# Performance work log

Measured on AMD Instinct MI355X. Metric: run time of the kernel, lower is better.

The kernel has to match this reference:

```python
import jax, jax.numpy as jnp
import numpy as np

B, H, W, C = 64, 14, 14, 768
HID = 4 * C            # ConvNeXt MLP hidden
E, K, R = 8, 2, 16     # num_experts, top_k, lora rank
SCALING = 16.0 / 16.0  # alpha / r


def setup_inputs() -> dict:
    key = jax.random.key(0)
    ks = jax.random.split(key, 9)
    N = B * H * W
    x = jax.random.normal(ks[0], (B, H, W, C), jnp.float32)
    p = jax.random.uniform(ks[1], (N, K), jnp.float32)
    topk_probs = p / (p.sum(-1, keepdims=True) + 1e-6)
    topk_idx = jax.random.randint(ks[2], (N, K), 0, E)
    w1 = jax.random.normal(ks[3], (C, HID), jnp.float32) * (C ** -0.5)
    b1 = jnp.zeros((HID,), jnp.float32)
    w2 = jax.random.normal(ks[4], (HID, C), jnp.float32) * (HID ** -0.5)
    b2 = jnp.zeros((C,), jnp.float32)
    w_down = jax.random.normal(ks[5], (E, C, R), jnp.float32) * (C ** -0.5)
    # torch init is zeros; use small randn so the op is numerically non-trivial
    w_up = jax.random.normal(ks[6], (E, R, C), jnp.float32) * 0.02
    return {"x": x, "topk_probs": topk_probs, "topk_idx": topk_idx,
            "w1": w1, "b1": b1, "w2": w2, "b2": b2,
            "w_down": w_down, "w_up": w_up}


def reference(x, topk_probs, topk_idx, w1, b1, w2, b2, w_down, w_up):
    # orig ConvNeXt MLP: Linear -> GELU(exact) -> Linear, pointwise over [B,H,W,C]
    h = jax.nn.gelu(jnp.einsum('bhwc,cf->bhwf', x, w1) + b1, approximate=False)
    orig = jnp.einsum('bhwf,fc->bhwc', h, w2) + b2

    N = x.shape[0] * x.shape[1] * x.shape[2]
    xf = x.reshape(N, C)  # [N, C] tokens
    # per-token combine weight for each expert: sum_k p[n,k] * 1[idx[n,k]==e]
    wt = (jax.nn.one_hot(topk_idx, E, dtype=xf.dtype) * topk_probs[..., None]).sum(1)  # [N, E]
    # dense-over-experts LoRA (vectorized form of the per-expert gather/scatter loop)
    down = jax.nn.gelu(jnp.einsum('nc,ecr->ner', xf, w_down), approximate=False)  # [N, E, R]
    up = jnp.einsum('ner,erc->nec', down, w_up) * SCALING                          # [N, E, C]
    moe = jnp.einsum('nec,ne->nc', up, wt)                                         # [N, C]
    return orig + moe.reshape(x.shape)
```

## Files before the change

### kernel.cpp

```cpp
#include <hip/hip_runtime.h>
#include <hip/hip_bf16.h>
#include <math.h>


#define NTOK   12544
#define CDIM   768
#define HIDDIM 3072
#define KBIG   3200

typedef __attribute__((ext_vector_type(8))) short bf16x8;
typedef __attribute__((ext_vector_type(4))) float f32x4;

#define GLOBAL_AS(p) ((const __attribute__((address_space(1))) void*)(p))
#define LDS_AS(p)    ((__attribute__((address_space(3))) void*)(p))
#define GLD(src, dst) __builtin_amdgcn_global_load_lds(GLOBAL_AS(src), LDS_AS(dst), 16, 0, 0)

__device__ inline unsigned short f2bf(float f) {
    unsigned int x = __float_as_uint(f);
    x += 0x7fffu + ((x >> 16) & 1u);
    return (unsigned short)(x >> 16);
}

__device__ inline float gelu_fast(float x) {
    float x3 = x * x * x;
    float u2 = 1.5957691216057308f * x + 0.07135481627260025f * x3;
    float e = __expf(-u2);
    return x * __builtin_amdgcn_rcpf(1.0f + e);
}

__global__ void __launch_bounds__(256) prep_kernel(
        const float* __restrict__ x, const float* __restrict__ w1,
        const float* __restrict__ w2, const float* __restrict__ wup,
        const float* __restrict__ wdn,
        unsigned short* __restrict__ xb, unsigned short* __restrict__ w1t,
        unsigned short* __restrict__ B2t, unsigned short* __restrict__ wdt) {
    __shared__ float tile[64][65];
    const int b = blockIdx.x, tid = threadIdx.x;
    if (b < 9408) {
        int i = b * 256 + tid;
        float4 v = ((const float4*)x)[i];
        ushort4 o;
        o.x = f2bf(v.x); o.y = f2bf(v.y); o.z = f2bf(v.z); o.w = f2bf(v.w);
        ((ushort4*)xb)[i] = o;
        return;
    }
    if (b < 10584) {
        const float* in; unsigned short* outp; int Ccols, out_ld, out_off, bx, by;
        if (b < 9984)       { int t = b - 9408;  in = w1;  outp = w1t; Ccols = 3072; out_ld = 768;  out_off = 0;    bx = t % 48; by = t / 48; }
        else if (b < 10560) { int t = b - 9984;  in = w2;  outp = B2t; Ccols = 768;  out_ld = 3200; out_off = 0;    bx = t % 12; by = t / 12; }
        else                { int t = b - 10560; in = wup; outp = B2t; Ccols = 768;  out_ld = 3200; out_off = 3072; bx = t % 12; by = t / 12; }
        const int c0 = bx * 64, r0 = by * 64;
        #pragma unroll
        for (int p = 0; p < 4; ++p) {
            int idx = p * 256 + tid;
            int r = idx >> 4, c4 = (idx & 15) * 4;
            float4 v = *(const float4*)&in[(size_t)(r0 + r) * Ccols + c0 + c4];
            tile[r][c4 + 0] = v.x; tile[r][c4 + 1] = v.y;
            tile[r][c4 + 2] = v.z; tile[r][c4 + 3] = v.w;
        }
        __syncthreads();
        #pragma unroll
        for (int p = 0; p < 2; ++p) {
            int u = p * 256 + tid;
            int cc = u >> 3, r8 = (u & 7) * 8;
            uint4 pk;
            pk.x = (unsigned)f2bf(tile[r8 + 0][cc]) | ((unsigned)f2bf(tile[r8 + 1][cc]) << 16);
            pk.y = (unsigned)f2bf(tile[r8 + 2][cc]) | ((unsigned)f2bf(tile[r8 + 3][cc]) << 16);
            pk.z = (unsigned)f2bf(tile[r8 + 4][cc]) | ((unsigned)f2bf(tile[r8 + 5][cc]) << 16);
            pk.w = (unsigned)f2bf(tile[r8 + 6][cc]) | ((unsigned)f2bf(tile[r8 + 7][cc]) << 16);
            *(uint4*)&outp[(size_t)(c0 + cc) * out_ld + out_off + r0 + r8] = pk;
        }
        return;
    }
    {
        int idx = (b - 10584) * 256 + tid;
        int j = idx / 768, c = idx - j * 768;
        int e = j >> 4, r = j & 15;
        wdt[idx] = f2bf(wdn[((size_t)e * 768 + c) * 16 + r]);
    }
}

template <int EPI, int TM>
__global__ void __launch_bounds__(TM * 2)
gemm_bt_kernel(const unsigned short* __restrict__ A, int lda,
               const unsigned short* __restrict__ Bt, int ldb,
               int kIters,
               const float* __restrict__ bias,
               unsigned short* __restrict__ apOut,
               float* __restrict__ fOut,
               const int* __restrict__ tki,
               const float* __restrict__ tkp) {
    constexpr int NT    = TM * 2;
    constexpr int ABUF  = TM * 32;
    constexpr int BBUF  = 128 * 32;
    __shared__ __align__(16) unsigned short As[2 * ABUF];
    __shared__ __align__(16) unsigned short Bs[2 * BBUF];

    const int bx = blockIdx.x, by = blockIdx.y;
    const int tid  = threadIdx.x;
    const int wave = tid >> 6;
    const int lane = tid & 63;
    const int m0 = by * TM;
    const int n0 = bx * 128;
    const int wm = (wave >> 1) * 64;
    const int wn = (wave & 1) * 64;
    const int row16 = lane & 15;
    const int quad  = lane >> 4;
    const int kch   = quad * 8;

    f32x4 acc[4][4] = {};

    const int r_s = tid >> 2;
    const int c_s = (tid & 3) * 8;
    const size_t aRow0 = (size_t)(m0 + r_s) * lda + c_s;
    const size_t aRow1 = aRow0 + (size_t)(NT / 4) * lda;
    const size_t bRow0 = (size_t)(n0 + r_s) * ldb + c_s;
    const size_t bRow1 = bRow0 + (size_t)64 * ldb;
    unsigned short* asB0 = &As[(wave * 64) * 8];
    unsigned short* asB1 = &As[(NT + wave * 64) * 8];
    unsigned short* bsB0 = &Bs[(wave * 64) * 8];
    unsigned short* bsB1 = &Bs[(256 + wave * 64) * 8];

    {
        GLD(A + aRow0, asB0);
        GLD(A + aRow1, asB1);
        GLD(Bt + bRow0, bsB0);
        if (TM == 128) GLD(Bt + bRow1, bsB1);
    }

    for (int kt = 0; kt < kIters; ++kt) {
        __syncthreads();

        if (kt + 1 < kIters) {
            const int k1 = (kt + 1) * 32;
            const int pa = ((kt + 1) & 1) * ABUF;
            const int pb = ((kt + 1) & 1) * BBUF;
            GLD(A + aRow0 + k1, asB0 + pa);
            GLD(A + aRow1 + k1, asB1 + pa);
            GLD(Bt + bRow0 + k1, bsB0 + pb);
            if (TM == 128) GLD(Bt + bRow1 + k1, bsB1 + pb);
        }

        const int ca = (kt & 1) * ABUF;
        const int cb = (kt & 1) * BBUF;
        bf16x8 af[4], bfr[4];
        #pragma unroll
        for (int mi = 0; mi < 4; ++mi)
            af[mi] = *(const bf16x8*)&As[ca + (wm + mi * 16 + row16) * 32 + kch];
        #pragma unroll
        for (int ni = 0; ni < 4; ++ni)
            bfr[ni] = *(const bf16x8*)&Bs[cb + (wn + ni * 16 + row16) * 32 + kch];

        #pragma unroll
        for (int mi = 0; mi < 4; ++mi)
            #pragma unroll
            for (int ni = 0; ni < 4; ++ni)
                acc[mi][ni] = __builtin_amdgcn_mfma_f32_16x16x32_bf16(
                    af[mi], bfr[ni], acc[mi][ni], 0, 0, 0);
    }

    #pragma unroll
    for (int mi = 0; mi < 4; ++mi) {
        #pragma unroll
        for (int i = 0; i < 4; ++i) {
            const int m = m0 + wm + mi * 16 + quad * 4 + i;
            int i0 = 0, i1 = 0; float p0 = 0.f, p1 = 0.f;
            if (EPI == 1) {
                i0 = tki[m * 2]; i1 = tki[m * 2 + 1];
                p0 = tkp[m * 2]; p1 = tkp[m * 2 + 1];
            }
            #pragma unroll
            for (int ni = 0; ni < 4; ++ni) {
                const int ncol = n0 + wn + ni * 16 + row16;
                float v = acc[mi][ni][i];
                if (EPI == 0) {
                    v = gelu_fast(v + bias[ncol]);
                    apOut[(size_t)m * KBIG + ncol] = f2bf(v);
                } else if (EPI == 1) {
                    const int e = ncol >> 4;
                    float wt = (i0 == e ? p0 : 0.f) + (i1 == e ? p1 : 0.f);
                    v = gelu_fast(v) * wt;
                    apOut[(size_t)m * KBIG + 3072 + ncol] = f2bf(v);
                } else {
                    fOut[(size_t)m * CDIM + ncol] = v + bias[ncol];
                }
            }
        }
    }
}


template <int P, bool TAILV, class Issue>
__device__ __forceinline__ void phase4(
        const char* lds, int aO0, int aO1, int bO0, int bO1,
        f32x4 (&acc)[4][3], bf16x8 (&bfr)[3][2], Issue issue) {
    bf16x8 af[2][2];
    #pragma unroll
    for (int f = 0; f < 2; ++f) {
        af[f][0] = *(const bf16x8*)(lds + aO0 + (2 * P + f) * 2048);
        af[f][1] = *(const bf16x8*)(lds + aO1 + (2 * P + f) * 2048);
    }
    if (P == 0) {
        #pragma unroll
        for (int nf = 0; nf < 3; ++nf) {
            bfr[nf][0] = *(const bf16x8*)(lds + bO0 + nf * 2048);
            bfr[nf][1] = *(const bf16x8*)(lds + bO1 + nf * 2048);
        }
    }
    issue();
    __builtin_amdgcn_s_barrier();
    asm volatile("s_waitcnt lgkmcnt(0)" ::: "memory");
    __builtin_amdgcn_sched_barrier(0);
    __builtin_amdgcn_s_setprio(1);
    #pragma unroll
    for (int f = 0; f < 2; ++f)
        #pragma unroll
        for (int nf = 0; nf < 3; ++nf)
            #pragma unroll
            for (int k = 0; k < 2; ++k)
                acc[2 * P + f][nf] = __builtin_amdgcn_mfma_f32_16x16x32_bf16(
                    af[f][k], bfr[nf][k], acc[2 * P + f][nf], 0, 0, 0);
    __builtin_amdgcn_s_setprio(0);
    if (TAILV) asm volatile("s_waitcnt vmcnt(3)" ::: "memory");
    __builtin_amdgcn_s_barrier();
    __builtin_amdgcn_sched_barrier(0);
}

template <int EPI, int NBX>
__global__ void __launch_bounds__(512, 4)
gemm4_kernel(const unsigned short* __restrict__ A, int lda,
             const unsigned short* __restrict__ Bt, int ldb,
             int kTiles, const float* __restrict__ bias,
             unsigned short* __restrict__ apOut, float* __restrict__ fOut) {
    __shared__ __align__(1024) char ldsraw[81920];
    char* ldsA = ldsraw;
    char* ldsB = ldsraw + 32768;

    const int nwg  = gridDim.x;
    const int q    = nwg >> 3, r = nwg & 7;
    const int orig = blockIdx.x;
    const int xcd  = orig & 7, within = orig >> 3;
    const int wgid = (xcd < r ? xcd * (q + 1) : r * (q + 1) + (xcd - r) * q) + within;
    const int bx = wgid % NBX, by = wgid / NBX;

    const int tid  = threadIdx.x;
    const int wave = tid >> 6;
    const int lane = tid & 63;
    const int m0 = by * 128;
    const int n0 = bx * 192;
    const int row16 = lane & 15;
    const int quad  = lane >> 4;
    const int wm = (wave >> 2) << 6;
    const int wn = (wave & 3) * 48;
    const int swz = (row16 & 7) << 4;
    const int aFB = ((wm + row16) << 7) + (quad << 4);
    const int bFB = ((wn + row16) << 7) + (quad << 4);
    const int aX0 = (aFB ^ swz),        aX1 = ((aFB + 64) ^ swz);
    const int bX0 = (bFB ^ swz) + 32768, bX1 = ((bFB + 64) ^ swz) + 32768;

    const int d  = tid << 4;
    const int s  = d ^ (((d >> 7) & 7) << 4);
    const int sr = s >> 7;
    const int sc = (s & 127) >> 1;
    const char* aSrc = (const char*)(A + (size_t)(m0 + sr) * lda + sc);
    const char* bSrc = (const char*)(Bt + (size_t)(n0 + sr) * ldb + sc);
    const size_t aStep = (size_t)64 * lda * 2;
    const size_t bStep = (size_t)64 * ldb * 2;
    const int ldsW = wave << 10;

    auto issueA = [&](int b, int tk) {
        const char* sp = aSrc + (size_t)tk * 128;
        char* dp = ldsA + b * 16384 + ldsW;
        GLD(sp, dp);
        GLD(sp + aStep, dp + 8192);
    };
    auto issueB = [&](int b, int tk) {
        const char* sp = bSrc + (size_t)tk * 128;
        char* dp = ldsB + b * 24576 + ldsW;
        GLD(sp, dp);
        GLD(sp + bStep, dp + 8192);
        GLD(sp + 2 * bStep, dp + 16384);
    };

    f32x4 acc[4][3] = {};

    issueB(0, 0);
    issueA(0, 0);
    issueB(1, 1);
    asm volatile("s_waitcnt vmcnt(3)" ::: "memory");
    __builtin_amdgcn_s_barrier();
    __builtin_amdgcn_sched_barrier(0);

    const int nIter = kTiles >> 1;
    for (int it = 0; it < nIter; ++it) {
        const int t  = it * 2;
        const int t2 = (t + 2 < kTiles) ? t + 2 : 0;
        const int t3 = (t + 3 < kTiles) ? t + 3 : 0;
        bf16x8 bfr[3][2];
        phase4<0, false>(ldsraw, aX0, aX1, bX0, bX1, acc, bfr,
                         [&]{ issueA(1, t + 1); });
        phase4<1, true >(ldsraw, aX0, aX1, bX0, bX1, acc, bfr,
                         [&]{ issueB(0, t2); });
        phase4<0, false>(ldsraw, aX0 + 16384, aX1 + 16384, bX0 + 24576, bX1 + 24576, acc, bfr,
                         [&]{ issueA(0, t2); });
        phase4<1, true >(ldsraw, aX0 + 16384, aX1 + 16384, bX0 + 24576, bX1 + 24576, acc, bfr,
                         [&]{ issueB(1, t3); });
    }
    asm volatile("s_waitcnt vmcnt(0)" ::: "memory");

    float bv[3];
    #pragma unroll
    for (int nf = 0; nf < 3; ++nf) bv[nf] = bias[n0 + wn + nf * 16 + row16];
    #pragma unroll
    for (int mi = 0; mi < 4; ++mi) {
        #pragma unroll
        for (int i = 0; i < 4; ++i) {
            const int m = m0 + wm + mi * 16 + quad * 4 + i;
            #pragma unroll
            for (int nf = 0; nf < 3; ++nf) {
                const int col = n0 + wn + nf * 16 + row16;
                float v = acc[mi][nf][i] + bv[nf];
                if (EPI == 0) apOut[(size_t)m * KBIG + col] = f2bf(gelu_fast(v));
                else          fOut[(size_t)m * CDIM + col] = v;
            }
        }
    }
}


extern "C" void kernel_launch(void* const* d_in, const int* in_sizes, int n_in,
                              void* d_out, int out_size, void* d_ws, size_t ws_size,
                              hipStream_t stream) {
    const float* x   = (const float*)d_in[0];
    const float* tkp = (const float*)d_in[1];
    const int*   tki = (const int*)d_in[2];
    const float* w1  = (const float*)d_in[3];
    const float* b1  = (const float*)d_in[4];
    const float* w2  = (const float*)d_in[5];
    const float* b2  = (const float*)d_in[6];
    const float* wdn = (const float*)d_in[7];
    const float* wup = (const float*)d_in[8];
    float* out = (float*)d_out;

    unsigned short* xb  = (unsigned short*)d_ws;
    unsigned short* w1t = xb  + (size_t)NTOK * CDIM;
    unsigned short* B2t = w1t + (size_t)HIDDIM * CDIM;
    unsigned short* wdt = B2t + (size_t)CDIM * KBIG;
    unsigned short* Ap  = wdt + (size_t)128 * CDIM;

    prep_kernel<<<dim3(10968), 256, 0, stream>>>(x, w1, w2, wup, wdn,
                                                 xb, w1t, B2t, wdt);

    gemm_bt_kernel<1, 128><<<dim3(1, NTOK / 128), 256, 0, stream>>>(
        xb, CDIM, wdt, CDIM, CDIM / 32, nullptr, Ap, nullptr, tki, tkp);
    gemm4_kernel<0, HIDDIM / 192><<<dim3((HIDDIM / 192) * (NTOK / 128)), 512, 0, stream>>>(
        xb, CDIM, w1t, CDIM, CDIM / 64, b1, Ap, nullptr);
    gemm4_kernel<2, CDIM / 192><<<dim3((CDIM / 192) * (NTOK / 128)), 512, 0, stream>>>(
        Ap, KBIG, B2t, KBIG, KBIG / 64, b2, nullptr, out);
}
```

Before: 264.2 us.

## Restructure main GEMMs to 256-thread blocks with K=32 tiles and larger per-wave N

Replaces the 512-thread, K=64-tile GEMM with a templated 256-thread version that uses 32-wide K tiles, 64-byte LDS rows with a new swizzle, and more N fragments per wave (6 for the first GEMM, 4 for the second, which now uses 128-wide N tiles). The aim is to lower the LDS footprint and raise occupancy while keeping per-wave MFMA work high. In exchange there are twice as many K iterations and barriers, and more accumulator registers per wave.

```diff
diff --git a/kernel.cpp b/kernel.cpp
--- a/kernel.cpp
+++ b/kernel.cpp
@@ -190,22 +190,17 @@
 }
 
 
-template <int P, bool TAILV, class Issue>
-__device__ __forceinline__ void phase4(
-        const char* lds, int aO0, int aO1, int bO0, int bO1,
-        f32x4 (&acc)[4][3], bf16x8 (&bfr)[3][2], Issue issue) {
-    bf16x8 af[2][2];
-    #pragma unroll
-    for (int f = 0; f < 2; ++f) {
-        af[f][0] = *(const bf16x8*)(lds + aO0 + (2 * P + f) * 2048);
-        af[f][1] = *(const bf16x8*)(lds + aO1 + (2 * P + f) * 2048);
-    }
+template <int NFRAG, int P, bool TAILV, class Issue>
+__device__ __forceinline__ void phase5(
+        const char* lds, int aO, int bO,
+        f32x4 (&acc)[4][NFRAG], bf16x8 (&bfr)[NFRAG], Issue issue) {
+    bf16x8 af[2];
+    af[0] = *(const bf16x8*)(lds + aO + (2 * P + 0) * 1024);
+    af[1] = *(const bf16x8*)(lds + aO + (2 * P + 1) * 1024);
     if (P == 0) {
         #pragma unroll
-        for (int nf = 0; nf < 3; ++nf) {
-            bfr[nf][0] = *(const bf16x8*)(lds + bO0 + nf * 2048);
-            bfr[nf][1] = *(const bf16x8*)(lds + bO1 + nf * 2048);
-        }
+        for (int nf = 0; nf < NFRAG; ++nf)
+            bfr[nf] = *(const bf16x8*)(lds + bO + nf * 1024);
     }
     issue();
     __builtin_amdgcn_s_barrier();
@@ -215,26 +210,29 @@
     #pragma unroll
     for (int f = 0; f < 2; ++f)
         #pragma unroll
-        for (int nf = 0; nf < 3; ++nf)
-            #pragma unroll
-            for (int k = 0; k < 2; ++k)
-                acc[2 * P + f][nf] = __builtin_amdgcn_mfma_f32_16x16x32_bf16(
-                    af[f][k], bfr[nf][k], acc[2 * P + f][nf], 0, 0, 0);
+        for (int nf = 0; nf < NFRAG; ++nf)
+            acc[2 * P + f][nf] = __builtin_amdgcn_mfma_f32_16x16x32_bf16(
+                af[f], bfr[nf], acc[2 * P + f][nf], 0, 0, 0);
     __builtin_amdgcn_s_setprio(0);
-    if (TAILV) asm volatile("s_waitcnt vmcnt(3)" ::: "memory");
+    if (TAILV) {
+        if constexpr (NFRAG == 6) asm volatile("s_waitcnt vmcnt(3)" ::: "memory");
+        else                      asm volatile("s_waitcnt vmcnt(2)" ::: "memory");
+    }
     __builtin_amdgcn_s_barrier();
     __builtin_amdgcn_sched_barrier(0);
 }
 
-template <int EPI, int NBX>
-__global__ void __launch_bounds__(512, 4)
-gemm4_kernel(const unsigned short* __restrict__ A, int lda,
+template <int EPI, int NFRAG, int NBX, int OCC>
+__global__ void __launch_bounds__(256, OCC)
+gemm5_kernel(const unsigned short* __restrict__ A, int lda,
              const unsigned short* __restrict__ Bt, int ldb,
              int kTiles, const float* __restrict__ bias,
              unsigned short* __restrict__ apOut, float* __restrict__ fOut) {
-    __shared__ __align__(1024) char ldsraw[81920];
+    constexpr int BBYTES = NFRAG * 2048;
+    constexpr int BCH    = NFRAG / 2;
+    __shared__ __align__(1024) char ldsraw[16384 + 2 * BBYTES];
     char* ldsA = ldsraw;
-    char* ldsB = ldsraw + 32768;
+    char* ldsB = ldsraw + 16384;
 
     const int nwg  = gridDim.x;
     const int q    = nwg >> 3, r = nwg & 7;
@@ -247,47 +245,46 @@
     const int wave = tid >> 6;
     const int lane = tid & 63;
     const int m0 = by * 128;
-    const int n0 = bx * 192;
+    const int n0 = bx * (NFRAG * 32);
     const int row16 = lane & 15;
     const int quad  = lane >> 4;
-    const int wm = (wave >> 2) << 6;
-    const int wn = (wave & 3) * 48;
-    const int swz = (row16 & 7) << 4;
-    const int aFB = ((wm + row16) << 7) + (quad << 4);
-    const int bFB = ((wn + row16) << 7) + (quad << 4);
-    const int aX0 = (aFB ^ swz),        aX1 = ((aFB + 64) ^ swz);
-    const int bX0 = (bFB ^ swz) + 32768, bX1 = ((bFB + 64) ^ swz) + 32768;
+    const int wm = (wave >> 1) * 64;
+    const int wn = (wave & 1) * (NFRAG * 16);
+    const int sw2 = (row16 >> 1) & 3;
+    const int aB = ((wm + row16) << 6) + ((quad ^ sw2) << 4);
+    const int bB = 16384 + ((wn + row16) << 6) + ((quad ^ sw2) << 4);
 
     const int d  = tid << 4;
-    const int s  = d ^ (((d >> 7) & 7) << 4);
-    const int sr = s >> 7;
-    const int sc = (s & 127) >> 1;
-    const char* aSrc = (const char*)(A + (size_t)(m0 + sr) * lda + sc);
-    const char* bSrc = (const char*)(Bt + (size_t)(n0 + sr) * ldb + sc);
-    const size_t aStep = (size_t)64 * lda * 2;
-    const size_t bStep = (size_t)64 * ldb * 2;
+    const int s  = d ^ (((d >> 7) & 3) << 4);
+    const int sr = s >> 6;
+    const int sc = (s & 63) >> 1;
+    const unsigned short* aSrc = A + (size_t)(m0 + sr) * lda + sc;
+    const unsigned short* bSrc = Bt + (size_t)(n0 + sr) * ldb + sc;
+    const size_t aStep = (size_t)64 * lda;
+    const size_t bStep = (size_t)64 * ldb;
     const int ldsW = wave << 10;
 
     auto issueA = [&](int b, int tk) {
-        const char* sp = aSrc + (size_t)tk * 128;
-        char* dp = ldsA + b * 16384 + ldsW;
+        const unsigned short* sp = aSrc + tk * 32;
+        char* dp = ldsA + b * 8192 + ldsW;
         GLD(sp, dp);
-        GLD(sp + aStep, dp + 8192);
+        GLD(sp + aStep, dp + 4096);
     };
     auto issueB = [&](int b, int tk) {
-        const char* sp = bSrc + (size_t)tk * 128;
-        char* dp = ldsB + b * 24576 + ldsW;
-        GLD(sp, dp);
-        GLD(sp + bStep, dp + 8192);
-        GLD(sp + 2 * bStep, dp + 16384);
+        const unsigned short* sp = bSrc + tk * 32;
+        char* dp = ldsB + b * BBYTES + ldsW;
+        #pragma unroll
+        for (int c = 0; c < BCH; ++c)
+            GLD(sp + (size_t)c * bStep, dp + c * 4096);
     };
 
-    f32x4 acc[4][3] = {};
+    f32x4 acc[4][NFRAG] = {};
 
     issueB(0, 0);
     issueA(0, 0);
     issueB(1, 1);
-    asm volatile("s_waitcnt vmcnt(3)" ::: "memory");
+    if constexpr (NFRAG == 6) asm volatile("s_waitcnt vmcnt(3)" ::: "memory");
+    else                      asm volatile("s_waitcnt vmcnt(2)" ::: "memory");
     __builtin_amdgcn_s_barrier();
     __builtin_amdgcn_sched_barrier(0);
 
@@ -296,28 +293,24 @@
         const int t  = it * 2;
         const int t2 = (t + 2 < kTiles) ? t + 2 : 0;
         const int t3 = (t + 3 < kTiles) ? t + 3 : 0;
-        bf16x8 bfr[3][2];
-        phase4<0, false>(ldsraw, aX0, aX1, bX0, bX1, acc, bfr,
-                         [&]{ issueA(1, t + 1); });
-        phase4<1, true >(ldsraw, aX0, aX1, bX0, bX1, acc, bfr,
-                         [&]{ issueB(0, t2); });
-        phase4<0, false>(ldsraw, aX0 + 16384, aX1 + 16384, bX0 + 24576, bX1 + 24576, acc, bfr,
-                         [&]{ issueA(0, t2); });
-        phase4<1, true >(ldsraw, aX0 + 16384, aX1 + 16384, bX0 + 24576, bX1 + 24576, acc, bfr,
-                         [&]{ issueB(1, t3); });
+        bf16x8 bfr[NFRAG];
+        phase5<NFRAG, 0, false>(ldsraw, aB, bB, acc, bfr, [&]{ issueA(1, t + 1); });
+        phase5<NFRAG, 1, true >(ldsraw, aB, bB, acc, bfr, [&]{ issueB(0, t2); });
+        phase5<NFRAG, 0, false>(ldsraw, aB + 8192, bB + BBYTES, acc, bfr, [&]{ issueA(0, t2); });
+        phase5<NFRAG, 1, true >(ldsraw, aB + 8192, bB + BBYTES, acc, bfr, [&]{ issueB(1, t3); });
     }
     asm volatile("s_waitcnt vmcnt(0)" ::: "memory");
 
-    float bv[3];
+    float bv[NFRAG];
     #pragma unroll
-    for (int nf = 0; nf < 3; ++nf) bv[nf] = bias[n0 + wn + nf * 16 + row16];
+    for (int nf = 0; nf < NFRAG; ++nf) bv[nf] = bias[n0 + wn + nf * 16 + row16];
     #pragma unroll
     for (int mi = 0; mi < 4; ++mi) {
         #pragma unroll
         for (int i = 0; i < 4; ++i) {
             const int m = m0 + wm + mi * 16 + quad * 4 + i;
             #pragma unroll
-            for (int nf = 0; nf < 3; ++nf) {
+            for (int nf = 0; nf < NFRAG; ++nf) {
                 const int col = n0 + wn + nf * 16 + row16;
                 float v = acc[mi][nf][i] + bv[nf];
                 if (EPI == 0) apOut[(size_t)m * KBIG + col] = f2bf(gelu_fast(v));
@@ -353,8 +346,10 @@
 
     gemm_bt_kernel<1, 128><<<dim3(1, NTOK / 128), 256, 0, stream>>>(
         xb, CDIM, wdt, CDIM, CDIM / 32, nullptr, Ap, nullptr, tki, tkp);
-    gemm4_kernel<0, HIDDIM / 192><<<dim3((HIDDIM / 192) * (NTOK / 128)), 512, 0, stream>>>(
-        xb, CDIM, w1t, CDIM, CDIM / 64, b1, Ap, nullptr);
-    gemm4_kernel<2, CDIM / 192><<<dim3((CDIM / 192) * (NTOK / 128)), 512, 0, stream>>>(
-        Ap, KBIG, B2t, KBIG, KBIG / 64, b2, nullptr, out);
-}
+    gemm5_kernel<0, 6, HIDDIM / 192, 3>
+        <<<dim3((HIDDIM / 192) * (NTOK / 128)), 256, 0, stream>>>(
+        xb, CDIM, w1t, CDIM, CDIM / 32, b1, Ap, nullptr);
+    gemm5_kernel<2, 4, CDIM / 128, 4>
+        <<<dim3((CDIM / 128) * (NTOK / 128)), 256, 0, stream>>>(
+        Ap, KBIG, B2t, KBIG, KBIG / 32, b2, nullptr, out);
+}
```

Result: slower. 292.3 us (+10.6%).

## Fold LoRA down-projection GEMM into first MLP GEMM launch as extra workgroups

Applied to the files above, without the earlier changes.

Removes the separate LoRA down-projection kernel launch and instead appends 98 extra workgroups to the first gemm4 launch. They compute xb·wdt (N=128) with the same swizzled, pipelined LDS/MFMA schedule, using 2 N-fragments per wave, and apply the gating-weighted GELU epilogue. This saves one launch and the slower non-pipelined kernel, and lets the LoRA tiles fill idle CUs at the tail of the main grid. The XCD remapping is simplified to assume the main block count divides by 8; if the trailing blocks are scheduled late they could lengthen the tail.

```diff
diff --git a/kernel.cpp b/kernel.cpp
--- a/kernel.cpp
+++ b/kernel.cpp
@@ -80,120 +80,10 @@
     }
 }
 
-template <int EPI, int TM>
-__global__ void __launch_bounds__(TM * 2)
-gemm_bt_kernel(const unsigned short* __restrict__ A, int lda,
-               const unsigned short* __restrict__ Bt, int ldb,
-               int kIters,
-               const float* __restrict__ bias,
-               unsigned short* __restrict__ apOut,
-               float* __restrict__ fOut,
-               const int* __restrict__ tki,
-               const float* __restrict__ tkp) {
-    constexpr int NT    = TM * 2;
-    constexpr int ABUF  = TM * 32;
-    constexpr int BBUF  = 128 * 32;
-    __shared__ __align__(16) unsigned short As[2 * ABUF];
-    __shared__ __align__(16) unsigned short Bs[2 * BBUF];
-
-    const int bx = blockIdx.x, by = blockIdx.y;
-    const int tid  = threadIdx.x;
-    const int wave = tid >> 6;
-    const int lane = tid & 63;
-    const int m0 = by * TM;
-    const int n0 = bx * 128;
-    const int wm = (wave >> 1) * 64;
-    const int wn = (wave & 1) * 64;
-    const int row16 = lane & 15;
-    const int quad  = lane >> 4;
-    const int kch   = quad * 8;
-
-    f32x4 acc[4][4] = {};
-
-    const int r_s = tid >> 2;
-    const int c_s = (tid & 3) * 8;
-    const size_t aRow0 = (size_t)(m0 + r_s) * lda + c_s;
-    const size_t aRow1 = aRow0 + (size_t)(NT / 4) * lda;
-    const size_t bRow0 = (size_t)(n0 + r_s) * ldb + c_s;
-    const size_t bRow1 = bRow0 + (size_t)64 * ldb;
-    unsigned short* asB0 = &As[(wave * 64) * 8];
-    unsigned short* asB1 = &As[(NT + wave * 64) * 8];
-    unsigned short* bsB0 = &Bs[(wave * 64) * 8];
-    unsigned short* bsB1 = &Bs[(256 + wave * 64) * 8];
-
-    {
-        GLD(A + aRow0, asB0);
-        GLD(A + aRow1, asB1);
-        GLD(Bt + bRow0, bsB0);
-        if (TM == 128) GLD(Bt + bRow1, bsB1);
-    }
-
-    for (int kt = 0; kt < kIters; ++kt) {
-        __syncthreads();
-
-        if (kt + 1 < kIters) {
-            const int k1 = (kt + 1) * 32;
-            const int pa = ((kt + 1) & 1) * ABUF;
-            const int pb = ((kt + 1) & 1) * BBUF;
-            GLD(A + aRow0 + k1, asB0 + pa);
-            GLD(A + aRow1 + k1, asB1 + pa);
-            GLD(Bt + bRow0 + k1, bsB0 + pb);
-            if (TM == 128) GLD(Bt + bRow1 + k1, bsB1 + pb);
-        }
-
-        const int ca = (kt & 1) * ABUF;
-        const int cb = (kt & 1) * BBUF;
-        bf16x8 af[4], bfr[4];
-        #pragma unroll
-        for (int mi = 0; mi < 4; ++mi)
-            af[mi] = *(const bf16x8*)&As[ca + (wm + mi * 16 + row16) * 32 + kch];
-        #pragma unroll
-        for (int ni = 0; ni < 4; ++ni)
-            bfr[ni] = *(const bf16x8*)&Bs[cb + (wn + ni * 16 + row16) * 32 + kch];
-
-        #pragma unroll
-        for (int mi = 0; mi < 4; ++mi)
-            #pragma unroll
-            for (int ni = 0; ni < 4; ++ni)
-                acc[mi][ni] = __builtin_amdgcn_mfma_f32_16x16x32_bf16(
-                    af[mi], bfr[ni], acc[mi][ni], 0, 0, 0);
-    }
-
-    #pragma unroll
-    for (int mi = 0; mi < 4; ++mi) {
-        #pragma unroll
-        for (int i = 0; i < 4; ++i) {
-            const int m = m0 + wm + mi * 16 + quad * 4 + i;
-            int i0 = 0, i1 = 0; float p0 = 0.f, p1 = 0.f;
-            if (EPI == 1) {
-                i0 = tki[m * 2]; i1 = tki[m * 2 + 1];
-                p0 = tkp[m * 2]; p1 = tkp[m * 2 + 1];
-            }
-            #pragma unroll
-            for (int ni = 0; ni < 4; ++ni) {
-                const int ncol = n0 + wn + ni * 16 + row16;
-                float v = acc[mi][ni][i];
-                if (EPI == 0) {
-                    v = gelu_fast(v + bias[ncol]);
-                    apOut[(size_t)m * KBIG + ncol] = f2bf(v);
-                } else if (EPI == 1) {
-                    const int e = ncol >> 4;
-                    float wt = (i0 == e ? p0 : 0.f) + (i1 == e ? p1 : 0.f);
-                    v = gelu_fast(v) * wt;
-                    apOut[(size_t)m * KBIG + 3072 + ncol] = f2bf(v);
-                } else {
-                    fOut[(size_t)m * CDIM + ncol] = v + bias[ncol];
-                }
-            }
-        }
-    }
-}
-
-
-template <int P, bool TAILV, class Issue>
-__device__ __forceinline__ void phase4(
+template <int NFRAG, int P, bool TAILV, int VMN, class Issue>
+__device__ __forceinline__ void phase4n(
         const char* lds, int aO0, int aO1, int bO0, int bO1,
-        f32x4 (&acc)[4][3], bf16x8 (&bfr)[3][2], Issue issue) {
+        f32x4 (&acc)[4][NFRAG], bf16x8 (&bfr)[NFRAG][2], Issue issue) {
     bf16x8 af[2][2];
     #pragma unroll
     for (int f = 0; f < 2; ++f) {
@@ -202,7 +92,7 @@
     }
     if (P == 0) {
         #pragma unroll
-        for (int nf = 0; nf < 3; ++nf) {
+        for (int nf = 0; nf < NFRAG; ++nf) {
             bfr[nf][0] = *(const bf16x8*)(lds + bO0 + nf * 2048);
             bfr[nf][1] = *(const bf16x8*)(lds + bO1 + nf * 2048);
         }
@@ -215,58 +105,130 @@
     #pragma unroll
     for (int f = 0; f < 2; ++f)
         #pragma unroll
-        for (int nf = 0; nf < 3; ++nf)
+        for (int nf = 0; nf < NFRAG; ++nf)
             #pragma unroll
             for (int k = 0; k < 2; ++k)
                 acc[2 * P + f][nf] = __builtin_amdgcn_mfma_f32_16x16x32_bf16(
                     af[f][k], bfr[nf][k], acc[2 * P + f][nf], 0, 0, 0);
     __builtin_amdgcn_s_setprio(0);
-    if (TAILV) asm volatile("s_waitcnt vmcnt(3)" ::: "memory");
+    if (TAILV) {
+        if constexpr (VMN == 3) asm volatile("s_waitcnt vmcnt(3)" ::: "memory");
+        else                    asm volatile("s_waitcnt vmcnt(2)" ::: "memory");
+    }
     __builtin_amdgcn_s_barrier();
     __builtin_amdgcn_sched_barrier(0);
 }
 
-template <int EPI, int NBX>
+template <int EPI, int NBX, bool LORA>
 __global__ void __launch_bounds__(512, 4)
 gemm4_kernel(const unsigned short* __restrict__ A, int lda,
              const unsigned short* __restrict__ Bt, int ldb,
              int kTiles, const float* __restrict__ bias,
-             unsigned short* __restrict__ apOut, float* __restrict__ fOut) {
+             unsigned short* __restrict__ apOut, float* __restrict__ fOut,
+             const int* __restrict__ tki, const float* __restrict__ tkp,
+             const unsigned short* __restrict__ Bt2) {
     __shared__ __align__(1024) char ldsraw[81920];
     char* ldsA = ldsraw;
     char* ldsB = ldsraw + 32768;
 
-    const int nwg  = gridDim.x;
-    const int q    = nwg >> 3, r = nwg & 7;
+    constexpr int MAIN = NBX * (NTOK / 128);
     const int orig = blockIdx.x;
-    const int xcd  = orig & 7, within = orig >> 3;
-    const int wgid = (xcd < r ? xcd * (q + 1) : r * (q + 1) + (xcd - r) * q) + within;
-    const int bx = wgid % NBX, by = wgid / NBX;
 
     const int tid  = threadIdx.x;
     const int wave = tid >> 6;
     const int lane = tid & 63;
-    const int m0 = by * 128;
-    const int n0 = bx * 192;
     const int row16 = lane & 15;
     const int quad  = lane >> 4;
     const int wm = (wave >> 2) << 6;
-    const int wn = (wave & 3) * 48;
     const int swz = (row16 & 7) << 4;
     const int aFB = ((wm + row16) << 7) + (quad << 4);
-    const int bFB = ((wn + row16) << 7) + (quad << 4);
-    const int aX0 = (aFB ^ swz),        aX1 = ((aFB + 64) ^ swz);
-    const int bX0 = (bFB ^ swz) + 32768, bX1 = ((bFB + 64) ^ swz) + 32768;
+    const int aX0 = (aFB ^ swz), aX1 = ((aFB + 64) ^ swz);
 
     const int d  = tid << 4;
     const int s  = d ^ (((d >> 7) & 7) << 4);
     const int sr = s >> 7;
     const int sc = (s & 127) >> 1;
+    const int ldsW = wave << 10;
+
+    if constexpr (LORA) {
+        if (orig >= MAIN) {
+            const int m0 = (orig - MAIN) * 128;
+            const int wn = (wave & 3) << 5;
+            const int bFB = ((wn + row16) << 7) + (quad << 4);
+            const int bX0 = (bFB ^ swz) + 32768, bX1 = ((bFB + 64) ^ swz) + 32768;
+            const char* aSrc = (const char*)(A + (size_t)(m0 + sr) * lda + sc);
+            const char* bSrc = (const char*)(Bt2 + (size_t)sr * CDIM + sc);
+            const size_t aStep = (size_t)64 * lda * 2;
+            const size_t bStep = (size_t)64 * CDIM * 2;
+            auto issueA = [&](int b, int tk) {
+                const char* sp = aSrc + (size_t)tk * 128;
+                char* dp = ldsA + b * 16384 + ldsW;
+                GLD(sp, dp);
+                GLD(sp + aStep, dp + 8192);
+            };
+            auto issueB = [&](int b, int tk) {
+                const char* sp = bSrc + (size_t)tk * 128;
+                char* dp = ldsB + b * 16384 + ldsW;
+                GLD(sp, dp);
+                GLD(sp + bStep, dp + 8192);
+            };
+            f32x4 acc[4][2] = {};
+            issueB(0, 0); issueA(0, 0); issueB(1, 1);
+            asm volatile("s_waitcnt vmcnt(2)" ::: "memory");
+            __builtin_amdgcn_s_barrier();
+            __builtin_amdgcn_sched_barrier(0);
+            const int nIter = kTiles >> 1;
+            for (int it = 0; it < nIter; ++it) {
+                const int t  = it * 2;
+                const int t2 = (t + 2 < kTiles) ? t + 2 : 0;
+                const int t3 = (t + 3 < kTiles) ? t + 3 : 0;
+                bf16x8 bfr[2][2];
+                phase4n<2, 0, false, 2>(ldsraw, aX0, aX1, bX0, bX1, acc, bfr,
+                                        [&]{ issueA(1, t + 1); });
+                phase4n<2, 1, true , 2>(ldsraw, aX0, aX1, bX0, bX1, acc, bfr,
+                                        [&]{ issueB(0, t2); });
+                phase4n<2, 0, false, 2>(ldsraw, aX0 + 16384, aX1 + 16384, bX0 + 16384, bX1 + 16384,
+                                        acc, bfr, [&]{ issueA(0, t2); });
+                phase4n<2, 1, true , 2>(ldsraw, aX0 + 16384, aX1 + 16384, bX0 + 16384, bX1 + 16384,
+                                        acc, bfr, [&]{ issueB(1, t3); });
+            }
+            asm volatile("s_waitcnt vmcnt(0)" ::: "memory");
+            #pragma unroll
+            for (int mi = 0; mi < 4; ++mi) {
+                #pragma unroll
+                for (int i = 0; i < 4; ++i) {
+                    const int m = m0 + wm + mi * 16 + quad * 4 + i;
+                    const int i0 = tki[m * 2], i1 = tki[m * 2 + 1];
+                    const float p0 = tkp[m * 2], p1 = tkp[m * 2 + 1];
+                    #pragma unroll
+                    for (int nf = 0; nf < 2; ++nf) {
+                        const int col = wn + nf * 16 + row16;
+                        const int e = col >> 4;
+                        float wt = (i0 == e ? p0 : 0.f) + (i1 == e ? p1 : 0.f);
+                        apOut[(size_t)m * KBIG + 3072 + col] =
+                            f2bf(gelu_fast(acc[mi][nf][i]) * wt);
+                    }
+                }
+            }
+            return;
+        }
+    }
+
+    constexpr int qq = MAIN / 8;
+    const int xcd = orig & 7, within = orig >> 3;
+    const int wgid = xcd * qq + within;
+    const int bx = wgid % NBX, by = wgid / NBX;
+
+    const int m0 = by * 128;
+    const int n0 = bx * 192;
+    const int wn = (wave & 3) * 48;
+    const int bFB = ((wn + row16) << 7) + (quad << 4);
+    const int bX0 = (bFB ^ swz) + 32768, bX1 = ((bFB + 64) ^ swz) + 32768;
+
     const char* aSrc = (const char*)(A + (size_t)(m0 + sr) * lda + sc);
     const char* bSrc = (const char*)(Bt + (size_t)(n0 + sr) * ldb + sc);
     const size_t aStep = (size_t)64 * lda * 2;
     const size_t bStep = (size_t)64 * ldb * 2;
-    const int ldsW = wave << 10;
 
     auto issueA = [&](int b, int tk) {
         const char* sp = aSrc + (size_t)tk * 128;
@@ -297,14 +259,14 @@
         const int t2 = (t + 2 < kTiles) ? t + 2 : 0;
         const int t3 = (t + 3 < kTiles) ? t + 3 : 0;
         bf16x8 bfr[3][2];
-        phase4<0, false>(ldsraw, aX0, aX1, bX0, bX1, acc, bfr,
-                         [&]{ issueA(1, t + 1); });
-        phase4<1, true >(ldsraw, aX0, aX1, bX0, bX1, acc, bfr,
-                         [&]{ issueB(0, t2); });
-        phase4<0, false>(ldsraw, aX0 + 16384, aX1 + 16384, bX0 + 24576, bX1 + 24576, acc, bfr,
-                         [&]{ issueA(0, t2); });
-        phase4<1, true >(ldsraw, aX0 + 16384, aX1 + 16384, bX0 + 24576, bX1 + 24576, acc, bfr,
-                         [&]{ issueB(1, t3); });
+        phase4n<3, 0, false, 3>(ldsraw, aX0, aX1, bX0, bX1, acc, bfr,
+                                [&]{ issueA(1, t + 1); });
+        phase4n<3, 1, true , 3>(ldsraw, aX0, aX1, bX0, bX1, acc, bfr,
+                                [&]{ issueB(0, t2); });
+        phase4n<3, 0, false, 3>(ldsraw, aX0 + 16384, aX1 + 16384, bX0 + 24576, bX1 + 24576,
+                                acc, bfr, [&]{ issueA(0, t2); });
+        phase4n<3, 1, true , 3>(ldsraw, aX0 + 16384, aX1 + 16384, bX0 + 24576, bX1 + 24576,
+                                acc, bfr, [&]{ issueB(1, t3); });
     }
     asm volatile("s_waitcnt vmcnt(0)" ::: "memory");
 
@@ -351,10 +313,10 @@
     prep_kernel<<<dim3(10968), 256, 0, stream>>>(x, w1, w2, wup, wdn,
                                                  xb, w1t, B2t, wdt);
 
-    gemm_bt_kernel<1, 128><<<dim3(1, NTOK / 128), 256, 0, stream>>>(
-        xb, CDIM, wdt, CDIM, CDIM / 32, nullptr, Ap, nullptr, tki, tkp);
-    gemm4_kernel<0, HIDDIM / 192><<<dim3((HIDDIM / 192) * (NTOK / 128)), 512, 0, stream>>>(
-        xb, CDIM, w1t, CDIM, CDIM / 64, b1, Ap, nullptr);
-    gemm4_kernel<2, CDIM / 192><<<dim3((CDIM / 192) * (NTOK / 128)), 512, 0, stream>>>(
-        Ap, KBIG, B2t, KBIG, KBIG / 64, b2, nullptr, out);
-}
+    gemm4_kernel<0, HIDDIM / 192, true>
+        <<<dim3((HIDDIM / 192 + 1) * (NTOK / 128)), 512, 0, stream>>>(
+        xb, CDIM, w1t, CDIM, CDIM / 64, b1, Ap, nullptr, tki, tkp, wdt);
+    gemm4_kernel<2, CDIM / 192, false>
+        <<<dim3((CDIM / 192) * (NTOK / 128)), 512, 0, stream>>>(
+        Ap, KBIG, B2t, KBIG, KBIG / 64, b2, nullptr, out, nullptr, nullptr, nullptr);
+}
```

After: 252.5 us. 4.4% less time.
